# Performance work log

Hardware: AMD Instinct MI355X
Metric: run time of the kernel (lower is better)

## Reference

```python
import jax, jax.numpy as jnp
import numpy as np
import math

N_HEADS, INPUT_DIM, EMBED_DIM = 8, 128, 128
KEY_DIM = EMBED_DIM // N_HEADS  # val_dim = key_dim = 16
B, N = 4, 512


def setup_inputs() -> dict:
    key = jax.random.key(0)
    ks = jax.random.split(key, 8)
    stdv_k = 1.0 / math.sqrt(KEY_DIM)
    stdv_e = 1.0 / math.sqrt(EMBED_DIM)
    stdv_1 = 1.0
    q = jax.random.normal(ks[0], (B, N, INPUT_DIM), dtype=jnp.float32)
    e = jax.random.normal(ks[1], (B, N, N, INPUT_DIM), dtype=jnp.float32)
    W_query = jax.random.uniform(ks[2], (N_HEADS, INPUT_DIM, KEY_DIM), jnp.float32, -stdv_k, stdv_k)
    W_key = jax.random.uniform(ks[3], (N_HEADS, INPUT_DIM, KEY_DIM), jnp.float32, -stdv_k, stdv_k)
    W_val = jax.random.uniform(ks[4], (N_HEADS, INPUT_DIM, KEY_DIM), jnp.float32, -stdv_k, stdv_k)
    E_val1 = jax.random.uniform(ks[5], (N_HEADS, INPUT_DIM, 1), jnp.float32, -stdv_1, stdv_1)
    W_out = jax.random.uniform(ks[6], (N_HEADS, KEY_DIM, EMBED_DIM), jnp.float32, -stdv_e, stdv_e)
    return {"q": q, "e": e, "W_query": W_query, "W_key": W_key,
            "W_val": W_val, "E_val1": E_val1, "W_out": W_out}


def reference(q, e, W_query, W_key, W_val, E_val1, W_out):
    # h = q (self-attention); shapes: q [B,N,D], e [B,N,N,D]
    norm = 1.0 / math.sqrt(W_query.shape[-1])
    Q = jnp.einsum('bnd,hdk->hbnk', q, W_query)  # [H,B,N,k]
    K = jnp.einsum('bnd,hdk->hbnk', q, W_key)
    V = jnp.einsum('bnd,hdv->hbnv', q, W_val)
    # edge bias: per-head scalar projection of edge features -> [H,B,N,N]
    E = jnp.einsum('bnmd,hd->hbnm', e, E_val1[..., 0])
    compat = norm * jnp.einsum('hbnk,hbmk->hbnm', Q, K) + E
    attn = jax.nn.softmax(compat, axis=-1)
    heads = jnp.einsum('hbnm,hbmv->hbnv', attn, V)
    out = jnp.einsum('hbnv,hve->bne', heads, W_out)  # [B,N,embed]
    return out
```

## Files before the change

kernel.cpp:

```cpp
#include <hip/hip_runtime.h>
#include <math.h>

#define BB 4
#define NN 512
#define DD 128
#define HH 8
#define KK 16

__global__ __launch_bounds__(128) void proj_kernel(
    const float* __restrict__ q,
    const float* __restrict__ Wq,
    const float* __restrict__ Wk,
    const float* __restrict__ Wv,
    float* __restrict__ Qs,
    float* __restrict__ Kp,
    float* __restrict__ Vp)
{
    __shared__ float qrow[DD];
    const int bn = blockIdx.x;
    const int t = threadIdx.x;
    qrow[t] = q[(size_t)bn * DD + t];
    __syncthreads();
    const int h = t >> 4;
    const int k = t & 15;
    const float* wq = Wq + (size_t)h * DD * KK + k;
    const float* wk = Wk + (size_t)h * DD * KK + k;
    const float* wv = Wv + (size_t)h * DD * KK + k;
    float aq = 0.f, ak = 0.f, av = 0.f;
#pragma unroll 16
    for (int d = 0; d < DD; ++d) {
        const float x = qrow[d];
        aq = fmaf(x, wq[(size_t)d * KK], aq);
        ak = fmaf(x, wk[(size_t)d * KK], ak);
        av = fmaf(x, wv[(size_t)d * KK], av);
    }
    Qs[(size_t)bn * DD + t] = aq * 0.25f;
    Kp[(size_t)bn * DD + t] = ak;
    Vp[(size_t)bn * DD + t] = av;
}

__global__ __launch_bounds__(256) void vt_kernel(
    const float* __restrict__ Vp, float* __restrict__ Vt)
{
    __shared__ float tile[64][129];
    const int b  = blockIdx.x >> 3;
    const int m0 = (blockIdx.x & 7) * 64;
    const int t  = threadIdx.x;
    const float* src = Vp + ((size_t)b * NN + m0) * DD;
#pragma unroll
    for (int j = 0; j < 8; ++j) {
        const int idx4 = t + j * 256;
        const float4 v = *(const float4*)(src + (size_t)idx4 * 4);
        const int r = idx4 >> 5, c = (idx4 & 31) * 4;
        tile[r][c] = v.x; tile[r][c+1] = v.y; tile[r][c+2] = v.z; tile[r][c+3] = v.w;
    }
    __syncthreads();
    const int m = t & 63;
#pragma unroll
    for (int p0 = 0; p0 < 128; p0 += 4) {
        const int p = p0 + (t >> 6);
        Vt[((size_t)b * DD + p) * NN + m0 + m] = tile[m][p];
    }
}

__global__ __launch_bounds__(256) void qkt_kernel(
    const float* __restrict__ Qs, const float* __restrict__ Kp,
    float* __restrict__ QKT)
{
    const int b    = blockIdx.x >> 7;
    const int n4   = blockIdx.x & 127;
    const int tid  = threadIdx.x;
    const int wave = tid >> 6;
    const int lane = tid & 63;
    const int sub  = lane >> 4;
    const int dc   = lane & 15;
    const int d0   = dc * 8;

    float qf[4][8];
#pragma unroll
    for (int j = 0; j < 4; ++j) {
        const float* qp = Qs + ((size_t)b * NN + n4 * 4 + j) * DD + d0;
        const float4 a = *(const float4*)qp;
        const float4 c = *(const float4*)(qp + 4);
        qf[j][0]=a.x; qf[j][1]=a.y; qf[j][2]=a.z; qf[j][3]=a.w;
        qf[j][4]=c.x; qf[j][5]=c.y; qf[j][6]=c.z; qf[j][7]=c.w;
    }
    const float* kbase = Kp + (size_t)b * NN * DD;
    for (int i = 0; i < 32; ++i) {
        const int m = wave * 128 + i * 4 + sub;
        const float* kp = kbase + (size_t)m * DD + d0;
        const float4 k0 = *(const float4*)kp;
        const float4 k1 = *(const float4*)(kp + 4);
        float kr[8];
        kr[0]=k0.x; kr[1]=k0.y; kr[2]=k0.z; kr[3]=k0.w;
        kr[4]=k1.x; kr[5]=k1.y; kr[6]=k1.z; kr[7]=k1.w;
#pragma unroll
        for (int j = 0; j < 4; ++j) {
            float s = kr[0] * qf[j][0];
#pragma unroll
            for (int u = 1; u < 8; ++u) s = fmaf(kr[u], qf[j][u], s);
            s += __shfl_xor(s, 1);
            if ((dc & 1) == 0)
                QKT[(((size_t)b * NN + n4 * 4 + j) * HH + (dc >> 1)) * NN + m] = s;
        }
    }
}

__global__ __launch_bounds__(256) void attn_kernel(
    const float* __restrict__ e,
    const float* __restrict__ Ev,
    const float* __restrict__ QKT,
    const float* __restrict__ Vt,
    const float* __restrict__ Wout,
    float* __restrict__ out)
{
    __shared__ float comp[HH][NN + 4];
    __shared__ float headsv[HH * KK];

    const int bn   = blockIdx.x;
    const int b    = bn >> 9;
    const int tid  = threadIdx.x;
    const int wave = tid >> 6;
    const int lane = tid & 63;
    const int sub  = lane >> 4;
    const int dc   = lane & 15;
    const int d0   = dc * 8;

    float ev[HH][8];
#pragma unroll
    for (int h = 0; h < HH; ++h) {
        const float4 a = *(const float4*)(Ev + h * DD + d0);
        const float4 c = *(const float4*)(Ev + h * DD + d0 + 4);
        ev[h][0]=a.x; ev[h][1]=a.y; ev[h][2]=a.z; ev[h][3]=a.w;
        ev[h][4]=c.x; ev[h][5]=c.y; ev[h][6]=c.z; ev[h][7]=c.w;
    }

    const bool hi8 = (dc & 8) != 0;
    const bool hi4 = (dc & 4) != 0;
    const bool hi2 = (dc & 2) != 0;
    const float* epl = e + (size_t)bn * NN * DD
                         + (size_t)(wave * 128 + sub) * DD + d0;

    auto do_pass = [&](const float4 e0, const float4 e1, const int p) {
        float er[8];
        er[0]=e0.x; er[1]=e0.y; er[2]=e0.z; er[3]=e0.w;
        er[4]=e1.x; er[5]=e1.y; er[6]=e1.z; er[7]=e1.w;
        float acc[HH];
#pragma unroll
        for (int h = 0; h < HH; ++h) {
            float s = er[0] * ev[h][0];
#pragma unroll
            for (int u = 1; u < 8; ++u) s = fmaf(er[u], ev[h][u], s);
            acc[h] = s;
        }
        float t4[4];
#pragma unroll
        for (int j = 0; j < 4; ++j) {
            const float keep = hi8 ? acc[j + 4] : acc[j];
            const float send = hi8 ? acc[j]     : acc[j + 4];
            t4[j] = keep + __shfl_xor(send, 8);
        }
        float t2[2];
#pragma unroll
        for (int j = 0; j < 2; ++j) {
            const float keep = hi4 ? t4[j + 2] : t4[j];
            const float send = hi4 ? t4[j]     : t4[j + 2];
            t2[j] = keep + __shfl_xor(send, 4);
        }
        float w;
        {
            const float keep = hi2 ? t2[1] : t2[0];
            const float send = hi2 ? t2[0] : t2[1];
            w = keep + __shfl_xor(send, 2);
        }
        w += __shfl_xor(w, 1);
        if ((dc & 1) == 0) comp[dc >> 1][wave * 128 + p * 4 + sub] = w;
    };

#define LDE(B0, B1, p) { const float* _p = epl + (size_t)(p) * 512; \
                         B0 = *(const float4*)_p; B1 = *(const float4*)(_p + 4); }

    float4 A0, A1, B0, B1, C0, C1;
    LDE(A0, A1, 0); LDE(B0, B1, 1);
    for (int p = 0; p < 30; p += 3) {
        LDE(C0, C1, p + 2); do_pass(A0, A1, p);
        LDE(A0, A1, p + 3); do_pass(B0, B1, p + 1);
        LDE(B0, B1, p + 4); do_pass(C0, C1, p + 2);
    }
    do_pass(A0, A1, 30); do_pass(B0, B1, 31);
#undef LDE
    __syncthreads();

#pragma unroll
    for (int hh = 0; hh < 2; ++hh) {
        const int h = wave * 2 + hh;
        const float* qk   = QKT + ((size_t)bn * HH + h) * NN;
        const float* vrow = Vt + ((size_t)b * DD + h * KK) * NN;

        float s[8];
#pragma unroll
        for (int i = 0; i < 8; ++i)
            s[i] = comp[h][lane + i * 64] + qk[lane + i * 64];

        float mx = s[0];
#pragma unroll
        for (int i = 1; i < 8; ++i) mx = fmaxf(mx, s[i]);
#pragma unroll
        for (int mask = 1; mask <= 32; mask <<= 1)
            mx = fmaxf(mx, __shfl_xor(mx, mask));

        float pr[8], psum = 0.f;
#pragma unroll
        for (int i = 0; i < 8; ++i) { pr[i] = __expf(s[i] - mx); psum += pr[i]; }

        float av[KK];
#pragma unroll
        for (int v = 0; v < KK; ++v) av[v] = 0.f;
#pragma unroll
        for (int v = 0; v < KK; ++v) {
            const float* vp = vrow + (size_t)v * NN + lane;
#pragma unroll
            for (int i = 0; i < 8; ++i)
                av[v] = fmaf(pr[i], vp[i * 64], av[v]);
        }
#pragma unroll
        for (int mask = 1; mask <= 32; mask <<= 1)
            psum += __shfl_xor(psum, mask);

        const bool s5 = (lane & 32) != 0;
        float a8[8];
#pragma unroll
        for (int j = 0; j < 8; ++j) {
            const float keep = s5 ? av[j + 8] : av[j];
            const float send = s5 ? av[j]     : av[j + 8];
            a8[j] = keep + __shfl_xor(send, 32);
        }
        const bool s4 = (lane & 16) != 0;
        float a4[4];
#pragma unroll
        for (int j = 0; j < 4; ++j) {
            const float keep = s4 ? a8[j + 4] : a8[j];
            const float send = s4 ? a8[j]     : a8[j + 4];
            a4[j] = keep + __shfl_xor(send, 16);
        }
        const bool s3 = (lane & 8) != 0;
        float a2[2];
#pragma unroll
        for (int j = 0; j < 2; ++j) {
            const float keep = s3 ? a4[j + 2] : a4[j];
            const float send = s3 ? a4[j]     : a4[j + 2];
            a2[j] = keep + __shfl_xor(send, 8);
        }
        const bool s2 = (lane & 4) != 0;
        float a1;
        {
            const float keep = s2 ? a2[1] : a2[0];
            const float send = s2 ? a2[0] : a2[1];
            a1 = keep + __shfl_xor(send, 4);
        }
        a1 += __shfl_xor(a1, 2);
        a1 += __shfl_xor(a1, 1);
        if ((lane & 3) == 0)
            headsv[h * KK + (lane >> 2)] = a1 / psum;
    }
    __syncthreads();

    if (tid < DD) {
        float o = 0.f;
#pragma unroll 8
        for (int p = 0; p < HH * KK; ++p)
            o = fmaf(headsv[p], Wout[(size_t)p * DD + tid], o);
        out[(size_t)bn * DD + tid] = o;
    }
}

extern "C" void kernel_launch(void* const* d_in, const int* in_sizes, int n_in,
                              void* d_out, int out_size, void* d_ws, size_t ws_size,
                              hipStream_t stream) {
    const float* q    = (const float*)d_in[0];
    const float* e    = (const float*)d_in[1];
    const float* Wq   = (const float*)d_in[2];
    const float* Wk   = (const float*)d_in[3];
    const float* Wv   = (const float*)d_in[4];
    const float* Ev   = (const float*)d_in[5];
    const float* Wout = (const float*)d_in[6];
    float* out = (float*)d_out;

    float* Qs  = (float*)d_ws;
    float* Kp  = Qs  + (size_t)BB * NN * DD;
    float* Vp  = Kp  + (size_t)BB * NN * DD;
    float* Vt  = Vp  + (size_t)BB * NN * DD;
    float* QKT = Vt  + (size_t)BB * DD * NN;

    proj_kernel<<<BB * NN, 128, 0, stream>>>(q, Wq, Wk, Wv, Qs, Kp, Vp);
    vt_kernel<<<BB * 8, 256, 0, stream>>>(Vp, Vt);
    qkt_kernel<<<BB * 128, 256, 0, stream>>>(Qs, Kp, QKT);
    attn_kernel<<<BB * NN, 256, 0, stream>>>(e, Ev, QKT, Vt, Wout, out);
}
```

Baseline: 200.7 us.

## Split edge-bias projection into separate streaming kernel with nontemporal loads

The fused attention kernel is split in two. The new ebias kernel streams the large edge tensor with nontemporal loads, using a global interleaved chunk mapping so each wave walks widely spaced 2KB chunks, and writes the per-head bias to a workspace buffer. A separate softmax kernel then reads that bias from global memory instead of shared memory. This aims to improve memory-bandwidth streaming of the dominant edge read, at the cost of an extra global write and read of a B*N*H*N bias tensor plus one more kernel launch.

Result: slower. 236.2 us (+17.7%).

```diff
diff --git a/kernel.cpp b/kernel.cpp
--- a/kernel.cpp
+++ b/kernel.cpp
@@ -6,6 +6,12 @@
 #define DD 128
 #define HH 8
 #define KK 16
+
+typedef float f4 __attribute__((ext_vector_type(4)));
+
+__device__ __forceinline__ f4 ntload4(const float* p) {
+    return __builtin_nontemporal_load(reinterpret_cast<const f4*>(p));
+}
 
 __global__ __launch_bounds__(128) void proj_kernel(
     const float* __restrict__ q,
@@ -106,25 +112,18 @@
     }
 }
 
-__global__ __launch_bounds__(256) void attn_kernel(
+__global__ __launch_bounds__(256) void ebias_kernel(
     const float* __restrict__ e,
     const float* __restrict__ Ev,
-    const float* __restrict__ QKT,
-    const float* __restrict__ Vt,
-    const float* __restrict__ Wout,
-    float* __restrict__ out)
-{
-    __shared__ float comp[HH][NN + 4];
-    __shared__ float headsv[HH * KK];
-
-    const int bn   = blockIdx.x;
-    const int b    = bn >> 9;
+    float* __restrict__ E)
+{
     const int tid  = threadIdx.x;
     const int wave = tid >> 6;
     const int lane = tid & 63;
     const int sub  = lane >> 4;
     const int dc   = lane & 15;
     const int d0   = dc * 8;
+    const int W    = blockIdx.x * 4 + wave;
 
     float ev[HH][8];
 #pragma unroll
@@ -134,14 +133,12 @@
         ev[h][0]=a.x; ev[h][1]=a.y; ev[h][2]=a.z; ev[h][3]=a.w;
         ev[h][4]=c.x; ev[h][5]=c.y; ev[h][6]=c.z; ev[h][7]=c.w;
     }
-
     const bool hi8 = (dc & 8) != 0;
     const bool hi4 = (dc & 4) != 0;
     const bool hi2 = (dc & 2) != 0;
-    const float* epl = e + (size_t)bn * NN * DD
-                         + (size_t)(wave * 128 + sub) * DD + d0;
-
-    auto do_pass = [&](const float4 e0, const float4 e1, const int p) {
+    const int laneoff = sub * DD + d0;
+
+    auto do_chunk = [&](const f4 e0, const f4 e1, const int C) {
         float er[8];
         er[0]=e0.x; er[1]=e0.y; er[2]=e0.z; er[3]=e0.w;
         er[4]=e1.x; er[5]=e1.y; er[6]=e1.z; er[7]=e1.w;
@@ -174,33 +171,52 @@
             w = keep + __shfl_xor(send, 2);
         }
         w += __shfl_xor(w, 1);
-        if ((dc & 1) == 0) comp[dc >> 1][wave * 128 + p * 4 + sub] = w;
+        if ((dc & 1) == 0) {
+            const int bn = C >> 7;
+            const int m  = ((C & 127) << 2) + sub;
+            E[((size_t)bn * HH + (dc >> 1)) * NN + m] = w;
+        }
     };
 
-#define LDE(B0, B1, p) { const float* _p = epl + (size_t)(p) * 512; \
-                         B0 = *(const float4*)_p; B1 = *(const float4*)(_p + 4); }
-
-    float4 A0, A1, B0, B1, C0, C1;
+#define LDE(B0, B1, p) { const float* _p = e + (size_t)(W + (p) * 8192) * 512 + laneoff; \
+                         B0 = ntload4(_p); B1 = ntload4(_p + 4); }
+
+    f4 A0, A1, B0, B1, C0, C1;
     LDE(A0, A1, 0); LDE(B0, B1, 1);
     for (int p = 0; p < 30; p += 3) {
-        LDE(C0, C1, p + 2); do_pass(A0, A1, p);
-        LDE(A0, A1, p + 3); do_pass(B0, B1, p + 1);
-        LDE(B0, B1, p + 4); do_pass(C0, C1, p + 2);
-    }
-    do_pass(A0, A1, 30); do_pass(B0, B1, 31);
+        LDE(C0, C1, p + 2); do_chunk(A0, A1, W + p * 8192);
+        LDE(A0, A1, p + 3); do_chunk(B0, B1, W + (p + 1) * 8192);
+        LDE(B0, B1, p + 4); do_chunk(C0, C1, W + (p + 2) * 8192);
+    }
+    do_chunk(A0, A1, W + 30 * 8192); do_chunk(B0, B1, W + 31 * 8192);
 #undef LDE
-    __syncthreads();
+}
+
+__global__ __launch_bounds__(256) void softmax_kernel(
+    const float* __restrict__ E,
+    const float* __restrict__ QKT,
+    const float* __restrict__ Vt,
+    const float* __restrict__ Wout,
+    float* __restrict__ out)
+{
+    __shared__ float headsv[HH * KK];
+    const int bn   = blockIdx.x;
+    const int b    = bn >> 9;
+    const int tid  = threadIdx.x;
+    const int wave = tid >> 6;
+    const int lane = tid & 63;
 
 #pragma unroll
     for (int hh = 0; hh < 2; ++hh) {
         const int h = wave * 2 + hh;
+        const float* eb   = E   + ((size_t)bn * HH + h) * NN;
         const float* qk   = QKT + ((size_t)bn * HH + h) * NN;
         const float* vrow = Vt + ((size_t)b * DD + h * KK) * NN;
 
         float s[8];
 #pragma unroll
         for (int i = 0; i < 8; ++i)
-            s[i] = comp[h][lane + i * 64] + qk[lane + i * 64];
+            s[i] = eb[lane + i * 64] + qk[lane + i * 64];
 
         float mx = s[0];
 #pragma unroll
@@ -291,9 +307,11 @@
     float* Vp  = Kp  + (size_t)BB * NN * DD;
     float* Vt  = Vp  + (size_t)BB * NN * DD;
     float* QKT = Vt  + (size_t)BB * DD * NN;
+    float* E   = QKT + (size_t)BB * NN * HH * NN;
 
     proj_kernel<<<BB * NN, 128, 0, stream>>>(q, Wq, Wk, Wv, Qs, Kp, Vp);
     vt_kernel<<<BB * 8, 256, 0, stream>>>(Vp, Vt);
     qkt_kernel<<<BB * 128, 256, 0, stream>>>(Qs, Kp, QKT);
-    attn_kernel<<<BB * NN, 256, 0, stream>>>(e, Ev, QKT, Vt, Wout, out);
-}
+    ebias_kernel<<<2048, 256, 0, stream>>>(e, Ev, E);
+    softmax_kernel<<<BB * NN, 256, 0, stream>>>(E, QKT, Vt, Wout, out);
+}
```
